# Kernel optimization log

Measured on AMD Instinct MI355X. Metric: run time of the kernel, lower is better.

The kernel has to match this reference:

```python
import jax, jax.numpy as jnp
import numpy as np

N, n, d = 4, 2048, 1024


def setup_inputs() -> dict:
    key = jax.random.key(0)
    k1, k2, k3, k4 = jax.random.split(key, 4)
    x = jax.random.normal(k1, (N, n, d), dtype=jnp.float32)
    mask = jax.random.randint(k2, (N, n, n), 0, 2, dtype=jnp.int32)
    Wqk = jax.random.normal(k3, (d, d), dtype=jnp.float32) * (d ** -0.5)
    Wvc = jax.random.normal(k4, (d, d), dtype=jnp.float32) * (d ** -0.5)
    return {"x": x, "mask": mask, "Wqk": Wqk, "Wvc": Wvc}


def reference(x, mask, Wqk, Wvc):
    # q = Wqk(x): torch Linear computes x @ W^T
    q = jnp.einsum('bnd,ed->bne', x, Wqk)          # [N, n, d]
    scale = jnp.asarray(x.shape[-1], x.dtype) ** 0.5
    scores = jnp.einsum('bnd,bmd->bnm', q, x) / scale  # [N, n, n]
    scores = jnp.where(mask == 0, jnp.asarray(-1e20, scores.dtype), scores)
    attention = jax.nn.softmax(scores, axis=-1)
    attended = jnp.einsum('bnm,bmd->bnd', attention, x)
    return jnp.einsum('bnd,ed->bne', attended, Wvc)
```

## Files before the change

kernel.cpp:

```cpp
#include <hip/hip_runtime.h>
#include <hip/hip_bf16.h>

typedef short bf16x8 __attribute__((ext_vector_type(8)));
typedef short s16x4  __attribute__((ext_vector_type(4)));
typedef short s16x8  __attribute__((ext_vector_type(8)));
typedef float f32x4  __attribute__((ext_vector_type(4)));

static __device__ __forceinline__ void async_cp16(const void* g, void* l) {
  __builtin_amdgcn_global_load_lds(
      (const __attribute__((address_space(1))) unsigned int*)g,
      (__attribute__((address_space(3))) unsigned int*)l, 16, 0, 0);
}

static __device__ __forceinline__ unsigned short f2bf_bits(float f) {
  union { __hip_bfloat16 b; unsigned short u; } cv;
  cv.b = __float2bfloat16(f);
  return cv.u;
}

#define BAR() __builtin_amdgcn_s_barrier()
#define LGKM0() do { asm volatile("s_waitcnt lgkmcnt(0)" ::: "memory"); __builtin_amdgcn_sched_barrier(0); } while (0)
#define VMW(n) do { asm volatile("s_waitcnt vmcnt(" #n ")" ::: "memory"); __builtin_amdgcn_sched_barrier(0); } while (0)

__global__ __launch_bounds__(256) void cvt_f32_to_bf16(const float* __restrict__ in,
                                                       __hip_bfloat16* __restrict__ out) {
  const long i = ((long)blockIdx.x * 256 + threadIdx.x) * 4;
  const float4 v = *(const float4*)(in + i);
  s16x4 o;
  o[0] = (short)f2bf_bits(v.x);
  o[1] = (short)f2bf_bits(v.y);
  o[2] = (short)f2bf_bits(v.z);
  o[3] = (short)f2bf_bits(v.w);
  *(s16x4*)(out + i) = o;
}

struct GemmDesc {
  const __hip_bfloat16* A; const __hip_bfloat16* B; void* C;
  int lda, ldb, ldc, mT, nT, tpb; long sA, sB, sC;
};

#define STAGE_A(bb, h, kt) do { \
  const __hip_bfloat16* sA0_ = Ab + aOff0 + (long)(h) * 64 * g.lda + (kt) * 64; \
  const __hip_bfloat16* sA1_ = Ab + aOff1 + (long)(h) * 64 * g.lda + (kt) * 64; \
  char* dA_ = lds + (bb) * 65536 + (h) * 16384 + t * 16; \
  async_cp16(sA0_, dA_); async_cp16(sA1_, dA_ + 8192); } while (0)

#define STAGE_B(bb, ks, kt) do { \
  const __hip_bfloat16* sB0_ = Bb + bOff0 + (kt) * 64 + (ks) * 32; \
  const __hip_bfloat16* sB1_ = Bb + bOff1 + (kt) * 64 + (ks) * 32; \
  char* dB_ = lds + (bb) * 65536 + 32768 + (ks) * 16384 + t * 16; \
  async_cp16(sB0_, dB_); async_cp16(sB1_, dB_ + 8192); } while (0)

#define PHASE(bb, mh, ks, READB, VM_STMT, ...) do { \
  if (READB) { \
    _Pragma("unroll") \
    for (int nf = 0; nf < 4; ++nf) \
      bq[nf] = *(const bf16x8*)(lds + (bb) * 65536 + 32768 + (ks) * 16384 + \
                (wn * 64 + nf * 16 + (lane & 15)) * 64 + (((lane >> 4) * 16) ^ bXor)); \
  } \
  _Pragma("unroll") \
  for (int mm = 0; mm < 4; ++mm) \
    af[mm] = *(const bf16x8*)(lds + (bb) * 65536 + (mh) * 16384 + \
              (wm * 64 + mm * 16 + (lane & 15)) * 128 + (((ks) * 64 + (lane >> 4) * 16) ^ aXor)); \
  __VA_ARGS__; \
  BAR(); \
  LGKM0(); \
  __builtin_amdgcn_s_setprio(1); \
  _Pragma("unroll") \
  for (int mm = 0; mm < 4; ++mm) \
    _Pragma("unroll") \
    for (int nf = 0; nf < 4; ++nf) \
      acc[(mh) * 4 + mm][nf] = \
        __builtin_amdgcn_mfma_f32_16x16x32_bf16(af[mm], bq[nf], acc[(mh) * 4 + mm][nf], 0, 0, 0); \
  __builtin_amdgcn_s_setprio(0); \
  VM_STMT; \
  BAR(); } while (0)

template<int MODE>
__global__ __launch_bounds__(512, 2) void gemm8(GemmDesc g0, GemmDesc g1, int nb0, int K) {
  __shared__ char lds[131072];
  const int bid = blockIdx.x, nwg = gridDim.x;
  const int wg = (bid & 7) * (nwg >> 3) + (bid >> 3);
  GemmDesc g = (wg < nb0) ? g0 : g1;
  const int id = (wg < nb0) ? wg : wg - nb0;
  const int bz = id / g.tpb;
  const int tl = id - bz * g.tpb;
  const int bm = tl / g.nT;
  const int bn = tl - bm * g.nT;
  const long m0 = (long)bm * 256, n0 = (long)bn * 256;
  const __hip_bfloat16* Ab = g.A + bz * g.sA;
  const __hip_bfloat16* Bb = g.B + bz * g.sB;
  const int t = threadIdx.x;
  const int lane = t & 63, w = t >> 6;
  const int wm = w >> 2, wn = w & 3;

  const int aR = t >> 3;
  const int aSlot = (t & 7) ^ (aR & 7);
  const long aOff0 = (m0 + aR) * (long)g.lda + aSlot * 8;
  const long aOff1 = (m0 + 128 + aR) * (long)g.lda + aSlot * 8;
  const int bR = t >> 2;
  const int bSlot = (t & 3) ^ ((t >> 3) & 3);
  const long bOff0 = (n0 + bR) * (long)g.ldb + bSlot * 8;
  const long bOff1 = (n0 + 128 + bR) * (long)g.ldb + bSlot * 8;
  const int aXor = (lane & 7) << 4;
  const int bXor = ((lane >> 1) & 3) << 4;

  f32x4 acc[8][4] = {};
  bf16x8 af[4], bq[4];

  const int nt = K >> 6;
  const int nJ = nt >> 1;

  STAGE_A(0, 0, 0); STAGE_A(0, 1, 0); STAGE_B(0, 0, 0); STAGE_B(0, 1, 0);
  STAGE_A(1, 0, 1); STAGE_B(1, 0, 1);
  VMW(4);
  BAR();

  for (int j = 0; j < nJ; ++j) {
    const int t0 = 2 * j, t1 = 2 * j + 1;
    const bool full = (j + 1 < nJ);
    PHASE(0, 0, 0, true,  {},                                    STAGE_A(1, 1, t1));
    PHASE(0, 1, 0, false, {},                                    STAGE_B(1, 1, t1));
    PHASE(0, 0, 1, true,  {},                                    if (full) STAGE_B(0, 0, t0 + 2));
    PHASE(0, 1, 1, false, { if (full) { VMW(4); } else { VMW(0); } },
                                                                 if (full) STAGE_A(0, 0, t0 + 2));
    PHASE(1, 0, 0, true,  {},                                    if (full) STAGE_A(0, 1, t0 + 2));
    PHASE(1, 1, 0, false, {},                                    if (full) STAGE_B(0, 1, t0 + 2));
    PHASE(1, 0, 1, true,  {},                                    if (full) STAGE_B(1, 0, t1 + 2));
    PHASE(1, 1, 1, false, { if (full) { VMW(4); } },             if (full) STAGE_A(1, 0, t1 + 2));
  }

  const long crow0 = m0 + wm * 128 + ((lane >> 4) * 4);
  const long ccol0 = n0 + wn * 64 + (lane & 15);
  if (MODE == 0) {
    float* C = (float*)g.C + bz * g.sC;
    #pragma unroll
    for (int m = 0; m < 8; ++m)
      #pragma unroll
      for (int nf = 0; nf < 4; ++nf)
        #pragma unroll
        for (int r = 0; r < 4; ++r)
          C[(crow0 + m * 16 + r) * g.ldc + ccol0 + nf * 16] = acc[m][nf][r];
  } else {
    __hip_bfloat16* C = (__hip_bfloat16*)g.C + bz * g.sC;
    #pragma unroll
    for (int m = 0; m < 8; ++m)
      #pragma unroll
      for (int nf = 0; nf < 4; ++nf)
        #pragma unroll
        for (int r = 0; r < 4; ++r)
          C[(crow0 + m * 16 + r) * g.ldc + ccol0 + nf * 16] = __float2bfloat16(acc[m][nf][r]);
  }
}

__global__ __launch_bounds__(256) void softmax_rows(float* __restrict__ S,
                                                    const int* __restrict__ Mask) {
  const long row = blockIdx.x;
  float* srow = S + row * 2048;
  const int* mrow = Mask + row * 2048;
  const int t = threadIdx.x;
  const float4 v0 = *(const float4*)(srow + t * 8);
  const float4 v1 = *(const float4*)(srow + t * 8 + 4);
  const int4 q0 = *(const int4*)(mrow + t * 8);
  const int4 q1 = *(const int4*)(mrow + t * 8 + 4);
  float f[8];
  f[0] = q0.x ? v0.x * 0.03125f : -1e20f;
  f[1] = q0.y ? v0.y * 0.03125f : -1e20f;
  f[2] = q0.z ? v0.z * 0.03125f : -1e20f;
  f[3] = q0.w ? v0.w * 0.03125f : -1e20f;
  f[4] = q1.x ? v1.x * 0.03125f : -1e20f;
  f[5] = q1.y ? v1.y * 0.03125f : -1e20f;
  f[6] = q1.z ? v1.z * 0.03125f : -1e20f;
  f[7] = q1.w ? v1.w * 0.03125f : -1e20f;

  float mx = f[0];
  #pragma unroll
  for (int i = 1; i < 8; ++i) mx = fmaxf(mx, f[i]);
  #pragma unroll
  for (int off = 32; off > 0; off >>= 1) mx = fmaxf(mx, __shfl_xor(mx, off));
  __shared__ float redm[4], reds[4];
  if ((t & 63) == 0) redm[t >> 6] = mx;
  __syncthreads();
  mx = fmaxf(fmaxf(redm[0], redm[1]), fmaxf(redm[2], redm[3]));

  float e[8];
  float s = 0.f;
  #pragma unroll
  for (int i = 0; i < 8; ++i) { e[i] = __expf(f[i] - mx); s += e[i]; }
  #pragma unroll
  for (int off = 32; off > 0; off >>= 1) s += __shfl_xor(s, off);
  if ((t & 63) == 0) reds[t >> 6] = s;
  __syncthreads();
  s = reds[0] + reds[1] + reds[2] + reds[3];
  const float inv = 1.f / s;

  __hip_bfloat16* prow = (__hip_bfloat16*)srow;
  s16x8 o;
  #pragma unroll
  for (int i = 0; i < 8; ++i) o[i] = (short)f2bf_bits(e[i] * inv);
  *(s16x8*)(prow + t * 8) = o;
}

extern "C" void kernel_launch(void* const* d_in, const int* in_sizes, int n_in,
                              void* d_out, int out_size, void* d_ws, size_t ws_size,
                              hipStream_t stream) {
  const float* x   = (const float*)d_in[0];
  const int*   msk = (const int*)d_in[1];
  const float* Wqk = (const float*)d_in[2];
  const float* Wvc = (const float*)d_in[3];
  float* out = (float*)d_out;
  char* ws = (char*)d_ws;

  __hip_bfloat16* xb   = (__hip_bfloat16*)(ws + 0);
  __hip_bfloat16* qb   = (__hip_bfloat16*)(ws + 16777216);
  __hip_bfloat16* vT   = (__hip_bfloat16*)(ws + 33554432);
  __hip_bfloat16* wqkb = (__hip_bfloat16*)(ws + 50331648);
  __hip_bfloat16* wvcb = (__hip_bfloat16*)(ws + 52428800);
  float*          S    = (float*)(ws + 54525952);

  cvt_f32_to_bf16<<<8192, 256, 0, stream>>>(x,   xb);
  cvt_f32_to_bf16<<<1024, 256, 0, stream>>>(Wqk, wqkb);
  cvt_f32_to_bf16<<<1024, 256, 0, stream>>>(Wvc, wvcb);

  GemmDesc gq{xb,   wqkb, qb, 1024, 1024, 1024, 32, 4, 128, 0L, 0L, 0L};
  GemmDesc gv{wvcb, xb,   vT, 1024, 1024, 2048,  4, 8,  32, 0L, 2097152L, 2097152L};
  gemm8<1><<<dim3(256), 512, 0, stream>>>(gq, gv, 128, 1024);

  GemmDesc gs{qb, xb, S, 1024, 1024, 2048, 8, 8, 64, 2097152L, 2097152L, 4194304L};
  gemm8<0><<<dim3(256), 512, 0, stream>>>(gs, gs, 256, 1024);

  softmax_rows<<<dim3(8192), 256, 0, stream>>>(S, msk);

  GemmDesc go{(const __hip_bfloat16*)S, vT, out, 4096, 2048, 1024, 8, 4, 32,
              8388608L, 2097152L, 2097152L};
  gemm8<0><<<dim3(128), 512, 0, stream>>>(go, go, 128, 2048);
}
```

Measured before the change: 167.8 us.

## Rewrite GEMM as templated 1024-thread triple-buffered kernel, store scores in bf16

The two-buffer, eight-phase 512-thread GEMM is replaced by a templated 1024-thread kernel with configurable BM/BK, a three-stage LDS ring and precomputed swizzled read offsets. The 1/sqrt(d) scale moves into the Q projection epilogue. The score matrix S is now written in bf16 rather than fp32, roughly halving the traffic for the scores write and the softmax read. The PV GEMM switches to 128-row tiles so it launches 256 blocks instead of 128. The trade-offs are extra rounding from bf16 scores and different occupancy and register pressure with 1024-thread blocks.

```diff
diff --git a/kernel.cpp b/kernel.cpp
--- a/kernel.cpp
+++ b/kernel.cpp
@@ -16,6 +16,11 @@
   union { __hip_bfloat16 b; unsigned short u; } cv;
   cv.b = __float2bfloat16(f);
   return cv.u;
+}
+static __device__ __forceinline__ float bf2f(short u) {
+  union { float f; unsigned v; } cv;
+  cv.v = ((unsigned)(unsigned short)u) << 16;
+  return cv.f;
 }
 
 #define BAR() __builtin_amdgcn_s_barrier()
@@ -36,142 +41,143 @@
 
 struct GemmDesc {
   const __hip_bfloat16* A; const __hip_bfloat16* B; void* C;
-  int lda, ldb, ldc, mT, nT, tpb; long sA, sB, sC;
+  int lda, ldb, ldc, nT, tpb; long sA, sB, sC; float cscale;
 };
 
-#define STAGE_A(bb, h, kt) do { \
-  const __hip_bfloat16* sA0_ = Ab + aOff0 + (long)(h) * 64 * g.lda + (kt) * 64; \
-  const __hip_bfloat16* sA1_ = Ab + aOff1 + (long)(h) * 64 * g.lda + (kt) * 64; \
-  char* dA_ = lds + (bb) * 65536 + (h) * 16384 + t * 16; \
-  async_cp16(sA0_, dA_); async_cp16(sA1_, dA_ + 8192); } while (0)
-
-#define STAGE_B(bb, ks, kt) do { \
-  const __hip_bfloat16* sB0_ = Bb + bOff0 + (kt) * 64 + (ks) * 32; \
-  const __hip_bfloat16* sB1_ = Bb + bOff1 + (kt) * 64 + (ks) * 32; \
-  char* dB_ = lds + (bb) * 65536 + 32768 + (ks) * 16384 + t * 16; \
-  async_cp16(sB0_, dB_); async_cp16(sB1_, dB_ + 8192); } while (0)
-
-#define PHASE(bb, mh, ks, READB, VM_STMT, ...) do { \
-  if (READB) { \
-    _Pragma("unroll") \
-    for (int nf = 0; nf < 4; ++nf) \
-      bq[nf] = *(const bf16x8*)(lds + (bb) * 65536 + 32768 + (ks) * 16384 + \
-                (wn * 64 + nf * 16 + (lane & 15)) * 64 + (((lane >> 4) * 16) ^ bXor)); \
-  } \
-  _Pragma("unroll") \
-  for (int mm = 0; mm < 4; ++mm) \
-    af[mm] = *(const bf16x8*)(lds + (bb) * 65536 + (mh) * 16384 + \
-              (wm * 64 + mm * 16 + (lane & 15)) * 128 + (((ks) * 64 + (lane >> 4) * 16) ^ aXor)); \
-  __VA_ARGS__; \
-  BAR(); \
-  LGKM0(); \
-  __builtin_amdgcn_s_setprio(1); \
-  _Pragma("unroll") \
-  for (int mm = 0; mm < 4; ++mm) \
-    _Pragma("unroll") \
-    for (int nf = 0; nf < 4; ++nf) \
-      acc[(mh) * 4 + mm][nf] = \
-        __builtin_amdgcn_mfma_f32_16x16x32_bf16(af[mm], bq[nf], acc[(mh) * 4 + mm][nf], 0, 0, 0); \
-  __builtin_amdgcn_s_setprio(0); \
-  VM_STMT; \
-  BAR(); } while (0)
-
-template<int MODE>
-__global__ __launch_bounds__(512, 2) void gemm8(GemmDesc g0, GemmDesc g1, int nb0, int K) {
-  __shared__ char lds[131072];
+template<int MODE, int BM_, int BK_>
+__global__ __launch_bounds__(1024, 4) void gemm16(GemmDesc g0, GemmDesc g1, int nb0, int K) {
+  constexpr int MR = BM_ / 64;
+  constexpr int KR = BK_ / 32;
+  constexpr int W  = BK_ * 2;
+  constexpr int NB = (256 * W) / 16384;
+  constexpr int BUFSZ = 16384 + NB * 16384;
+  constexpr int KW = 1 + NB;
+  __shared__ char lds[3 * BUFSZ];
+
   const int bid = blockIdx.x, nwg = gridDim.x;
   const int wg = (bid & 7) * (nwg >> 3) + (bid >> 3);
   GemmDesc g = (wg < nb0) ? g0 : g1;
   const int id = (wg < nb0) ? wg : wg - nb0;
-  const int bz = id / g.tpb;
-  const int tl = id - bz * g.tpb;
-  const int bm = tl / g.nT;
-  const int bn = tl - bm * g.nT;
-  const long m0 = (long)bm * 256, n0 = (long)bn * 256;
+  const int bz = id / g.tpb, tl = id - bz * g.tpb;
+  const int bm = tl / g.nT, bn = tl - bm * g.nT;
+  const long m0 = (long)bm * BM_, n0 = (long)bn * 256;
   const __hip_bfloat16* Ab = g.A + bz * g.sA;
   const __hip_bfloat16* Bb = g.B + bz * g.sB;
+
   const int t = threadIdx.x;
   const int lane = t & 63, w = t >> 6;
   const int wm = w >> 2, wn = w & 3;
-
-  const int aR = t >> 3;
-  const int aSlot = (t & 7) ^ (aR & 7);
-  const long aOff0 = (m0 + aR) * (long)g.lda + aSlot * 8;
-  const long aOff1 = (m0 + 128 + aR) * (long)g.lda + aSlot * 8;
-  const int bR = t >> 2;
-  const int bSlot = (t & 3) ^ ((t >> 3) & 3);
-  const long bOff0 = (n0 + bR) * (long)g.ldb + bSlot * 8;
-  const long bOff1 = (n0 + 128 + bR) * (long)g.ldb + bSlot * 8;
-  const int aXor = (lane & 7) << 4;
-  const int bXor = ((lane >> 1) & 3) << 4;
-
-  f32x4 acc[8][4] = {};
-  bf16x8 af[4], bq[4];
-
-  const int nt = K >> 6;
-  const int nJ = nt >> 1;
-
-  STAGE_A(0, 0, 0); STAGE_A(0, 1, 0); STAGE_B(0, 0, 0); STAGE_B(0, 1, 0);
-  STAGE_A(1, 0, 1); STAGE_B(1, 0, 1);
-  VMW(4);
+  const int lr = lane & 15, cs = lane >> 4;
+
+  const int rA  = t / (W / 16);
+  const int dsl = t % (W / 16);
+  const int ssl = dsl ^ ((W == 64) ? ((rA >> 1) & 3) : (rA & 7));
+  const __hip_bfloat16* aSt  = Ab + (m0 + rA) * g.lda + ssl * 8;
+  const __hip_bfloat16* bSt0 = Bb + (n0 + rA) * g.ldb + ssl * 8;
+  const __hip_bfloat16* bSt1 = Bb + (n0 + 128 + rA) * g.ldb + ssl * 8;
+
+  const int axor = (W == 64) ? (((lr >> 1) & 3) << 4) : ((lr & 7) << 4);
+  int aRd[MR][KR], bRd[4][KR];
+  #pragma unroll
+  for (int mm = 0; mm < MR; ++mm)
+    #pragma unroll
+    for (int ks = 0; ks < KR; ++ks)
+      aRd[mm][ks] = (wm * (BM_ / 4) + mm * 16 + lr) * W + ((((ks * 4 + cs) << 4) ^ axor));
+  #pragma unroll
+  for (int nf = 0; nf < 4; ++nf)
+    #pragma unroll
+    for (int ks = 0; ks < KR; ++ks)
+      bRd[nf][ks] = 16384 + (wn * 64 + nf * 16 + lr) * W + ((((ks * 4 + cs) << 4) ^ axor));
+
+  f32x4 acc[MR][4] = {};
+
+  #define STAGE(kt, base) do { \
+    async_cp16(aSt + (long)(kt) * BK_, lds + (base) + t * 16); \
+    async_cp16(bSt0 + (long)(kt) * BK_, lds + (base) + 16384 + t * 16); \
+    if (NB == 2) async_cp16(bSt1 + (long)(kt) * BK_, lds + (base) + 32768 + t * 16); \
+  } while (0)
+  #define VM_KW() do { if constexpr (KW == 2) { VMW(2); } else { VMW(3); } } while (0)
+
+  const int nt = K / BK_;
+  STAGE(0, 0);
+  STAGE(1, BUFSZ);
+  VM_KW();
   BAR();
 
-  for (int j = 0; j < nJ; ++j) {
-    const int t0 = 2 * j, t1 = 2 * j + 1;
-    const bool full = (j + 1 < nJ);
-    PHASE(0, 0, 0, true,  {},                                    STAGE_A(1, 1, t1));
-    PHASE(0, 1, 0, false, {},                                    STAGE_B(1, 1, t1));
-    PHASE(0, 0, 1, true,  {},                                    if (full) STAGE_B(0, 0, t0 + 2));
-    PHASE(0, 1, 1, false, { if (full) { VMW(4); } else { VMW(0); } },
-                                                                 if (full) STAGE_A(0, 0, t0 + 2));
-    PHASE(1, 0, 0, true,  {},                                    if (full) STAGE_A(0, 1, t0 + 2));
-    PHASE(1, 1, 0, false, {},                                    if (full) STAGE_B(0, 1, t0 + 2));
-    PHASE(1, 0, 1, true,  {},                                    if (full) STAGE_B(1, 0, t1 + 2));
-    PHASE(1, 1, 1, false, { if (full) { VMW(4); } },             if (full) STAGE_A(1, 0, t1 + 2));
+  int rb = 0, sb = 2 * BUFSZ;
+  for (int tt = 0; tt < nt; ++tt) {
+    bf16x8 af[MR][KR], bq[4][KR];
+    #pragma unroll
+    for (int mm = 0; mm < MR; ++mm)
+      #pragma unroll
+      for (int ks = 0; ks < KR; ++ks)
+        af[mm][ks] = *(const bf16x8*)(lds + rb + aRd[mm][ks]);
+    #pragma unroll
+    for (int nf = 0; nf < 4; ++nf)
+      #pragma unroll
+      for (int ks = 0; ks < KR; ++ks)
+        bq[nf][ks] = *(const bf16x8*)(lds + rb + bRd[nf][ks]);
+    if (tt + 2 < nt) STAGE(tt + 2, sb);
+    LGKM0();
+    __builtin_amdgcn_s_setprio(1);
+    #pragma unroll
+    for (int ks = 0; ks < KR; ++ks)
+      #pragma unroll
+      for (int mm = 0; mm < MR; ++mm)
+        #pragma unroll
+        for (int nf = 0; nf < 4; ++nf)
+          acc[mm][nf] = __builtin_amdgcn_mfma_f32_16x16x32_bf16(af[mm][ks], bq[nf][ks], acc[mm][nf], 0, 0, 0);
+    __builtin_amdgcn_s_setprio(0);
+    if (tt + 2 < nt) { VM_KW(); } else { VMW(0); }
+    BAR();
+    rb = (rb == 2 * BUFSZ) ? 0 : rb + BUFSZ;
+    sb = (sb == 2 * BUFSZ) ? 0 : sb + BUFSZ;
   }
-
-  const long crow0 = m0 + wm * 128 + ((lane >> 4) * 4);
-  const long ccol0 = n0 + wn * 64 + (lane & 15);
+  #undef STAGE
+  #undef VM_KW
+
+  const long crow0 = m0 + wm * (BM_ / 4) + cs * 4;
+  const long ccol0 = n0 + wn * 64 + lr;
   if (MODE == 0) {
     float* C = (float*)g.C + bz * g.sC;
     #pragma unroll
-    for (int m = 0; m < 8; ++m)
+    for (int mm = 0; mm < MR; ++mm)
       #pragma unroll
       for (int nf = 0; nf < 4; ++nf)
         #pragma unroll
-        for (int r = 0; r < 4; ++r)
-          C[(crow0 + m * 16 + r) * g.ldc + ccol0 + nf * 16] = acc[m][nf][r];
+        for (int rr = 0; rr < 4; ++rr)
+          C[(crow0 + mm * 16 + rr) * g.ldc + ccol0 + nf * 16] = acc[mm][nf][rr];
   } else {
     __hip_bfloat16* C = (__hip_bfloat16*)g.C + bz * g.sC;
     #pragma unroll
-    for (int m = 0; m < 8; ++m)
+    for (int mm = 0; mm < MR; ++mm)
       #pragma unroll
       for (int nf = 0; nf < 4; ++nf)
         #pragma unroll
-        for (int r = 0; r < 4; ++r)
-          C[(crow0 + m * 16 + r) * g.ldc + ccol0 + nf * 16] = __float2bfloat16(acc[m][nf][r]);
+        for (int rr = 0; rr < 4; ++rr)
+          C[(crow0 + mm * 16 + rr) * g.ldc + ccol0 + nf * 16] =
+              __float2bfloat16(acc[mm][nf][rr] * g.cscale);
   }
 }
 
-__global__ __launch_bounds__(256) void softmax_rows(float* __restrict__ S,
+__global__ __launch_bounds__(256) void softmax_rows(__hip_bfloat16* __restrict__ S,
                                                     const int* __restrict__ Mask) {
   const long row = blockIdx.x;
-  float* srow = S + row * 2048;
+  short* srow = (short*)(S + row * 2048);
   const int* mrow = Mask + row * 2048;
   const int t = threadIdx.x;
-  const float4 v0 = *(const float4*)(srow + t * 8);
-  const float4 v1 = *(const float4*)(srow + t * 8 + 4);
+  const s16x8 sv = *(const s16x8*)(srow + t * 8);
   const int4 q0 = *(const int4*)(mrow + t * 8);
   const int4 q1 = *(const int4*)(mrow + t * 8 + 4);
   float f[8];
-  f[0] = q0.x ? v0.x * 0.03125f : -1e20f;
-  f[1] = q0.y ? v0.y * 0.03125f : -1e20f;
-  f[2] = q0.z ? v0.z * 0.03125f : -1e20f;
-  f[3] = q0.w ? v0.w * 0.03125f : -1e20f;
-  f[4] = q1.x ? v1.x * 0.03125f : -1e20f;
-  f[5] = q1.y ? v1.y * 0.03125f : -1e20f;
-  f[6] = q1.z ? v1.z * 0.03125f : -1e20f;
-  f[7] = q1.w ? v1.w * 0.03125f : -1e20f;
+  f[0] = q0.x ? bf2f(sv[0]) : -1e20f;
+  f[1] = q0.y ? bf2f(sv[1]) : -1e20f;
+  f[2] = q0.z ? bf2f(sv[2]) : -1e20f;
+  f[3] = q0.w ? bf2f(sv[3]) : -1e20f;
+  f[4] = q1.x ? bf2f(sv[4]) : -1e20f;
+  f[5] = q1.y ? bf2f(sv[5]) : -1e20f;
+  f[6] = q1.z ? bf2f(sv[6]) : -1e20f;
+  f[7] = q1.w ? bf2f(sv[7]) : -1e20f;
 
   float mx = f[0];
   #pragma unroll
@@ -194,11 +200,10 @@
   s = reds[0] + reds[1] + reds[2] + reds[3];
   const float inv = 1.f / s;
 
-  __hip_bfloat16* prow = (__hip_bfloat16*)srow;
   s16x8 o;
   #pragma unroll
   for (int i = 0; i < 8; ++i) o[i] = (short)f2bf_bits(e[i] * inv);
-  *(s16x8*)(prow + t * 8) = o;
+  *(s16x8*)(srow + t * 8) = o;
 }
 
 extern "C" void kernel_launch(void* const* d_in, const int* in_sizes, int n_in,
@@ -216,22 +221,21 @@
   __hip_bfloat16* vT   = (__hip_bfloat16*)(ws + 33554432);
   __hip_bfloat16* wqkb = (__hip_bfloat16*)(ws + 50331648);
   __hip_bfloat16* wvcb = (__hip_bfloat16*)(ws + 52428800);
-  float*          S    = (float*)(ws + 54525952);
+  __hip_bfloat16* Sbf  = (__hip_bfloat16*)(ws + 54525952);
 
   cvt_f32_to_bf16<<<8192, 256, 0, stream>>>(x,   xb);
   cvt_f32_to_bf16<<<1024, 256, 0, stream>>>(Wqk, wqkb);
   cvt_f32_to_bf16<<<1024, 256, 0, stream>>>(Wvc, wvcb);
 
-  GemmDesc gq{xb,   wqkb, qb, 1024, 1024, 1024, 32, 4, 128, 0L, 0L, 0L};
-  GemmDesc gv{wvcb, xb,   vT, 1024, 1024, 2048,  4, 8,  32, 0L, 2097152L, 2097152L};
-  gemm8<1><<<dim3(256), 512, 0, stream>>>(gq, gv, 128, 1024);
-
-  GemmDesc gs{qb, xb, S, 1024, 1024, 2048, 8, 8, 64, 2097152L, 2097152L, 4194304L};
-  gemm8<0><<<dim3(256), 512, 0, stream>>>(gs, gs, 256, 1024);
-
-  softmax_rows<<<dim3(8192), 256, 0, stream>>>(S, msk);
-
-  GemmDesc go{(const __hip_bfloat16*)S, vT, out, 4096, 2048, 1024, 8, 4, 32,
-              8388608L, 2097152L, 2097152L};
-  gemm8<0><<<dim3(128), 512, 0, stream>>>(go, go, 128, 2048);
-}
+  GemmDesc gq{xb,   wqkb, qb, 1024, 1024, 1024, 4, 128, 0L, 0L, 0L, 0.03125f};
+  GemmDesc gv{wvcb, xb,   vT, 1024, 1024, 2048, 8, 32, 0L, 2097152L, 2097152L, 1.f};
+  gemm16<1, 256, 32><<<dim3(256), 1024, 0, stream>>>(gq, gv, 128, 1024);
+
+  GemmDesc gs{qb, xb, Sbf, 1024, 1024, 2048, 8, 64, 2097152L, 2097152L, 4194304L, 1.f};
+  gemm16<1, 256, 32><<<dim3(256), 1024, 0, stream>>>(gs, gs, 256, 1024);
+
+  softmax_rows<<<dim3(8192), 256, 0, stream>>>(Sbf, msk);
+
+  GemmDesc go{Sbf, vT, out, 2048, 2048, 1024, 4, 64, 4194304L, 2097152L, 2097152L, 1.f};
+  gemm16<0, 128, 64><<<dim3(256), 1024, 0, stream>>>(go, go, 256, 2048);
+}
```

Measured after the change: 144.5 us. 13.9% less time.
